# Optimization experiments

Hardware: AMD Instinct MI355X
Metric: run time of the kernel (lower is better)

Reference implementation:

```python
import jax, jax.numpy as jnp
import numpy as np

B, C, H, W = 16, 3, 512, 512
TH, TW = 32, 32  # template h, w


def setup_inputs() -> dict:
    key = jax.random.key(0)
    k1, k2 = jax.random.split(key)
    im = jax.random.normal(k1, (B, C, H, W), dtype=jnp.float32)
    template = jax.random.normal(k2, (B, C, TH, TW), dtype=jnp.float32)
    return {"im": im, "template": template}


def _integral(x):
    # double cumsum -> integral image
    return jnp.cumsum(jnp.cumsum(x, axis=-1), axis=-2)


def _rect_sum(int_im, out_h, out_w, rh, rw):
    # Sum over rh x rw rectangles centered on each pixel. Because the gather
    # indices in the torch code form contiguous ranges, advanced indexing
    # reduces to 4 static slices of the integral image.
    return (int_im[..., :out_h, :out_w] + int_im[..., rh:, rw:]
            - int_im[..., :out_h, rw:] - int_im[..., rh:, :out_w])


def _ncc(im, template):
    Hh, Ww = im.shape[-2], im.shape[-1]
    th, tw = template.shape[-2], template.shape[-1]
    padWl = (tw - 1) // 2
    padWr = padWl + 1 - tw % 2
    padHt = (th - 1) // 2
    padHb = padHt + 1 - th % 2
    rh = padHt + padHb + 1  # rectangle height (== th for even th)
    rw = padWl + padWr + 1
    pad2d = ((0, 0), (0, 0), (padHt + 1, padHb), (padWl + 1, padWr))

    # local-mean centering via integral image
    rect = _rect_sum(_integral(jnp.pad(im, pad2d)), Hh, Ww, rh, rw)
    im_c = im - rect / (th * tw)
    t_c = template - template.mean(axis=(-2, -1), keepdims=True)

    # local energy via second integral image over squared centered image
    rect2 = _rect_sum(_integral(jnp.pad(im_c * im_c, pad2d)), Hh, Ww, rh, rw)
    energy = jnp.sqrt(jnp.clip(rect2, 0.0))
    t_norm = jnp.sqrt(jnp.sum(t_c * t_c, axis=(-2, -1), keepdims=True))

    # FFT cross-correlation (padding='same')
    ph = Hh + th - th % 2 - Hh % 2
    pw = Ww + tw - tw % 2 - Ww % 2
    f_im = jnp.fft.rfft2(im_c / energy, s=(ph, pw))
    f_t = jnp.fft.rfft2(jnp.flip(t_c / t_norm, axis=(-2, -1)), s=(ph, pw))
    full = jnp.fft.irfft2(f_im * f_t, s=(ph, pw))
    hH, hW = th // 2, tw // 2
    return full[..., hH:hH + Hh, hW:hW + Ww]


def reference(im, template):
    return _ncc(im, template)
```

## Files before the change

kernel.cpp:

```cpp
#include <hip/hip_runtime.h>
#include <hip/hip_bf16.h>
#include <math.h>

#define HH 512
#define WW 512
#define BC 48
#define GW 544
#define GH 545
#define PST (GH * GW)

#define ROWB 384
#define COPYSTRIDE 6208
#define BUFSTRIDE (2 * COPYSTRIDE)
#define LDSBYTES (2 * BUFSTRIDE)

#define SIMS 98

typedef __bf16 v8bf __attribute__((ext_vector_type(8)));
typedef float v16f __attribute__((ext_vector_type(16)));

__global__ __launch_bounds__(256) void k_template(const float* __restrict__ t,
                                                  __hip_bfloat16* __restrict__ tn)
{
    __shared__ float red[256];
    const int bc = blockIdx.x, tid = threadIdx.x;
    const float* tp = t + bc * 1024;
    float v0 = tp[tid], v1 = tp[tid + 256], v2 = tp[tid + 512], v3 = tp[tid + 768];
    red[tid] = v0 + v1 + v2 + v3;
    __syncthreads();
    for (int sft = 128; sft > 0; sft >>= 1) {
        if (tid < sft) red[tid] += red[tid + sft];
        __syncthreads();
    }
    float mean = red[0] * (1.0f / 1024.0f);
    __syncthreads();
    float c0 = v0 - mean, c1 = v1 - mean, c2 = v2 - mean, c3 = v3 - mean;
    red[tid] = c0 * c0 + c1 * c1 + c2 * c2 + c3 * c3;
    __syncthreads();
    for (int sft = 128; sft > 0; sft >>= 1) {
        if (tid < sft) red[tid] += red[tid + sft];
        __syncthreads();
    }
    float norm = sqrtf(red[0]);
    __hip_bfloat16* o = tn + bc * 1024;
    o[tid] = __float2bfloat16(c0 / norm);
    o[tid + 256] = __float2bfloat16(c1 / norm);
    o[tid + 512] = __float2bfloat16(c2 / norm);
    o[tid + 768] = __float2bfloat16(c3 / norm);
}

__global__ __launch_bounds__(256) void k_center2(const float* __restrict__ im,
                                                 __hip_bfloat16* __restrict__ T0)
{
    __shared__ __hip_bfloat16 sim[159 * SIMS];
    __shared__ float hs[159 * 64];
    const int j0 = blockIdx.x * 64;
    const int i0 = blockIdx.y * 128;
    const int plane = blockIdx.z;
    const int tid = threadIdx.x;
    const size_t iplane = (size_t)plane * HH * WW;
    const size_t gplane = (size_t)plane * PST;

    for (int k = tid; k < 159 * 96; k += 256) {
        int r = k / 96, c = k - r * 96;
        int gi = i0 + r - 15, gj = j0 + c - 16;
        float v = (gi >= 0 && gi < HH && gj >= 0 && gj < WW)
                      ? im[iplane + (size_t)gi * WW + gj] : 0.f;
        sim[r * SIMS + c] = __float2bfloat16(v);
    }
    __syncthreads();

    if (tid < 159) {
        const __hip_bfloat16* sr = sim + tid * SIMS;
        float s0 = 0.f;
#pragma unroll
        for (int c = 1; c <= 32; c++) s0 += __bfloat162float(sr[c]);
        hs[tid * 64] = s0;
        for (int j = 1; j < 64; j++) {
            s0 += __bfloat162float(sr[j + 32]) - __bfloat162float(sr[j]);
            hs[tid * 64 + j] = s0;
        }
    }
    __syncthreads();

    const int tc = tid & 63;
    const int lr0 = (tid >> 6) * 32;
    float run = 0.f;
#pragma unroll
    for (int d = 0; d < 32; d++) run += hs[(lr0 + d) * 64 + tc];
    for (int rr = 0; rr < 32; rr++) {
        int lr = lr0 + rr;
        int gi = i0 + lr;
        float imv = __bfloat162float(sim[(lr + 15) * SIMS + tc + 16]);
        float val = imv - run * (1.0f / 1024.0f);
        T0[gplane + (size_t)(16 + gi) * GW + 16 + j0 + tc] = __float2bfloat16(val);
        if (rr < 31) run += hs[(lr + 32) * 64 + tc] - hs[lr * 64 + tc];
    }
    if (blockIdx.x == 0) {
        for (int k = tid; k < 128 * 16; k += 256) {
            int rr = k >> 4, x = k & 15;
            T0[gplane + (size_t)(16 + i0 + rr) * GW + x] = __float2bfloat16(0.f);
        }
    }
    if (blockIdx.x == 7) {
        for (int k = tid; k < 128 * 16; k += 256) {
            int rr = k >> 4, x = k & 15;
            T0[gplane + (size_t)(16 + i0 + rr) * GW + 528 + x] = __float2bfloat16(0.f);
        }
    }
    if (blockIdx.x == 0 && blockIdx.y == 0) {
        for (int k = tid; k < 16 * GW; k += 256)
            T0[gplane + k] = __float2bfloat16(0.f);
    }
    if (blockIdx.x == 0 && blockIdx.y == 3) {
        size_t b = gplane + (size_t)528 * GW;
        for (int k = tid; k < 17 * GW; k += 256)
            T0[b + k] = __float2bfloat16(0.f);
    }
}

__global__ __launch_bounds__(256) void k_norm2(const __hip_bfloat16* __restrict__ T0,
                                               __hip_bfloat16* __restrict__ G0,
                                               __hip_bfloat16* __restrict__ G1)
{
    __shared__ __hip_bfloat16 sim[159 * SIMS];
    __shared__ float hs[159 * 64];
    const int j0 = blockIdx.x * 64;
    const int i0 = blockIdx.y * 128;
    const int plane = blockIdx.z;
    const int tid = threadIdx.x;
    const size_t gplane = (size_t)plane * PST;

    for (int k = tid; k < 159 * 96; k += 256) {
        int r = k / 96, c = k - r * 96;
        sim[r * SIMS + c] = T0[gplane + (size_t)(i0 + 1 + r) * GW + j0 + c];
    }
    __syncthreads();

    if (tid < 159) {
        const __hip_bfloat16* sr = sim + tid * SIMS;
        float s0 = 0.f;
#pragma unroll
        for (int c = 1; c <= 32; c++) {
            float v = __bfloat162float(sr[c]);
            s0 += v * v;
        }
        hs[tid * 64] = s0;
        for (int j = 1; j < 64; j++) {
            float a = __bfloat162float(sr[j + 32]);
            float b = __bfloat162float(sr[j]);
            s0 += a * a - b * b;
            hs[tid * 64 + j] = s0;
        }
    }
    __syncthreads();

    const int tc = tid & 63;
    const int lr0 = (tid >> 6) * 32;
    float run = 0.f;
#pragma unroll
    for (int d = 0; d < 32; d++) run += hs[(lr0 + d) * 64 + tc];
    for (int rr = 0; rr < 32; rr++) {
        int lr = lr0 + rr;
        int gi = i0 + lr;
        int c = j0 + tc;
        float e = sqrtf(fmaxf(run, 0.f));
        float v = __bfloat162float(sim[(lr + 15) * SIMS + tc + 16]) / e;
        __hip_bfloat16 w = __float2bfloat16(v);
        size_t pr = gplane + (size_t)(16 + gi) * GW;
        G0[pr + 16 + c] = w;
        G1[pr + 15 + c] = w;
        if (rr < 31) run += hs[(lr + 32) * 64 + tc] - hs[lr * 64 + tc];
    }
    if (blockIdx.x == 0) {
        for (int k = tid; k < 128 * 16; k += 256) {
            int rr = k >> 4, x = k & 15;
            size_t pr = gplane + (size_t)(16 + i0 + rr) * GW;
            G0[pr + x] = __float2bfloat16(0.f);
            if (x < 15) G1[pr + x] = __float2bfloat16(0.f);
        }
    }
    if (blockIdx.x == 7) {
        for (int k = tid; k < 128 * 17; k += 256) {
            int rr = k / 17, x = k % 17;
            size_t pr = gplane + (size_t)(16 + i0 + rr) * GW;
            G1[pr + 527 + x] = __float2bfloat16(0.f);
            if (x > 0) G0[pr + 527 + x] = __float2bfloat16(0.f);
        }
    }
    if (blockIdx.x == 0 && blockIdx.y == 0) {
        for (int k = tid; k < 16 * GW; k += 256) {
            G0[gplane + k] = __float2bfloat16(0.f);
            G1[gplane + k] = __float2bfloat16(0.f);
        }
    }
    if (blockIdx.x == 0 && blockIdx.y == 3) {
        size_t b = gplane + (size_t)528 * GW;
        for (int k = tid; k < 17 * GW; k += 256) {
            G0[b + k] = __float2bfloat16(0.f);
            G1[b + k] = __float2bfloat16(0.f);
        }
    }
}

template <int PHASE>
__device__ __forceinline__ void compute_chunk(const unsigned int* __restrict__ Lr,
                                              v8bf a0, v8bf a1,
                                              float (&C)[16],
                                              int h, int Tbase, int i0,
                                              float* outp)
{
#pragma unroll
    for (int t = 0; t < 16; ++t) {
        const unsigned int* p = Lr + PHASE * (BUFSTRIDE / 4) + t * (ROWB / 4);
        union { unsigned int u[4]; v8bf v; } B0, B1;
        B0.u[0] = p[0];  B0.u[1] = p[1];  B0.u[2] = p[2];  B0.u[3] = p[3];
        B1.u[0] = p[8];  B1.u[1] = p[9];  B1.u[2] = p[10]; B1.u[3] = p[11];
        v16f c;
#pragma unroll
        for (int q = 0; q < 16; ++q) c[q] = C[q];
        c = __builtin_amdgcn_mfma_f32_32x32x16_bf16(a1, B1.v, c, 0, 0, 0);
        c = __builtin_amdgcn_mfma_f32_32x32x16_bf16(a0, B0.v, c, 0, 0, 0);
        const int T = Tbase + t;
        if (T >= 31 && T <= 94) {
            if (h) {
                const int ret = i0 - 31 + T;
                outp[(size_t)ret * WW] = c[15];
            }
        }
        float t3  = __shfl_xor(c[3], 32);
        float t7  = __shfl_xor(c[7], 32);
        float t11 = __shfl_xor(c[11], 32);
        float t15 = __shfl_xor(c[15], 32);
        C[0]  = h ? t3  : 0.f;
        C[4]  = h ? t7  : t3;
        C[8]  = h ? t11 : t7;
        C[12] = h ? t15 : t11;
#pragma unroll
        for (int g = 0; g < 4; ++g)
#pragma unroll
            for (int k = 1; k < 4; ++k)
                C[4 * g + k] = c[4 * g + k - 1];
    }
}

__global__ __launch_bounds__(256) void k_corr_mfma(const __hip_bfloat16* __restrict__ G0,
                                                   const __hip_bfloat16* __restrict__ G1,
                                                   const __hip_bfloat16* __restrict__ Tn,
                                                   float* __restrict__ out)
{
    __shared__ __align__(16) char lds[LDSBYTES];
    const int tid = threadIdx.x;
    const int wid = tid >> 6;
    const int lane = tid & 63;
    const int n = lane & 31;
    const int h = lane >> 5;
    const int j0 = blockIdx.x * 128;
    const int j0w = j0 + wid * 32;
    const int i0 = blockIdx.y * 64;
    const int plane = blockIdx.z;

    const v8bf* tp = (const v8bf*)(Tn + (size_t)plane * 1024 + n * 32 + 8 * h);
    const v8bf a0 = tp[0];
    const v8bf a1 = tp[2];

    const int c0 = j0w + n - 15 + 8 * h;
    const int sel = c0 & 1;
    const int dbase = (32 * wid + n + 1 + 8 * h - sel) >> 1;
    const unsigned int* Lr = (const unsigned int*)(lds + sel * COPYSTRIDE) + dbase;

    const __hip_bfloat16* g0p = G0 + (size_t)plane * PST + (size_t)(i0 + 1) * GW + j0;
    const __hip_bfloat16* g1p = G1 + (size_t)plane * PST + (size_t)(i0 + 1) * GW + j0;

    const __hip_bfloat16* srcp[3];
    int ldso[3];
#pragma unroll
    for (int k = 0; k < 3; ++k) {
        int s = wid + 4 * k;
        int cp = (s >= 6) ? 1 : 0;
        int c2 = cp ? (s - 6) : s;
        int q = c2 * 1024 + lane * 16;
        int rl = q / ROWB;
        int cb = q - rl * ROWB;
        srcp[k] = (cp ? g1p : g0p) + rl * GW + (cb >> 1);
        ldso[k] = cp * COPYSTRIDE + c2 * 1024;
    }

    float C[16];
#pragma unroll
    for (int s = 0; s < 16; s++) C[s] = 0.f;

    float* outp = out + (size_t)plane * HH * WW + j0w + n;

    auto stage = [&](int R, int b) {
#pragma unroll
        for (int k = 0; k < 3; ++k) {
            __builtin_amdgcn_global_load_lds(
                (const __attribute__((address_space(1))) void*)(srcp[k] + (size_t)R * GW),
                (__attribute__((address_space(3))) void*)(lds + b * BUFSTRIDE + ldso[k]),
                16, 0, 0);
        }
    };

    stage(0, 0);
    stage(16, 1);
    __syncthreads();

    for (int k2 = 0; k2 < 3; ++k2) {
        compute_chunk<0>(Lr, a0, a1, C, h, 32 * k2, i0, outp);
        __syncthreads();
        if (k2 < 2) stage(32 * k2 + 32, 0);
        compute_chunk<1>(Lr, a0, a1, C, h, 32 * k2 + 16, i0, outp);
        __syncthreads();
        if (k2 < 2) stage(32 * k2 + 48, 1);
    }
}

extern "C" void kernel_launch(void* const* d_in, const int* in_sizes, int n_in,
                              void* d_out, int out_size, void* d_ws, size_t ws_size,
                              hipStream_t stream)
{
    const float* im = (const float*)d_in[0];
    const float* tmpl = (const float*)d_in[1];
    float* outp = (float*)d_out;
    __hip_bfloat16* T0 = (__hip_bfloat16*)d_out;
    __hip_bfloat16* G0 = (__hip_bfloat16*)d_ws;
    __hip_bfloat16* G1 = G0 + (size_t)BC * PST;
    __hip_bfloat16* Tn = G1 + (size_t)BC * PST;

    k_template<<<48, 256, 0, stream>>>(tmpl, Tn);
    k_center2<<<dim3(8, 4, BC), 256, 0, stream>>>(im, T0);
    k_norm2<<<dim3(8, 4, BC), 256, 0, stream>>>(T0, G0, G1);
    k_corr_mfma<<<dim3(4, 8, BC), 256, 0, stream>>>(G0, G1, Tn, outp);
}
```

Measured before the change: 299.6 us.

## Replace LDS staging in MFMA correlation with direct global register prefetch

The correlation kernel no longer stages image rows into shared memory with global_load_lds and block barriers. Each lane now loads its B-operand vectors straight from global memory into a rotating register ring six rows deep, fully unrolled over the 96 rows. This removes LDS traffic and __syncthreads stalls, at the cost of more VGPRs and redundant, possibly unaligned global/L2 reads across overlapping lanes.

Result: no change. 303.4 us (+1.3%).

```diff
diff --git a/kernel.cpp b/kernel.cpp
--- a/kernel.cpp
+++ b/kernel.cpp
@@ -8,11 +8,6 @@
 #define GW 544
 #define GH 545
 #define PST (GH * GW)
-
-#define ROWB 384
-#define COPYSTRIDE 6208
-#define BUFSTRIDE (2 * COPYSTRIDE)
-#define LDSBYTES (2 * BUFSTRIDE)
 
 #define SIMS 98
 
@@ -203,25 +198,59 @@
     }
 }
 
-template <int PHASE>
-__device__ __forceinline__ void compute_chunk(const unsigned int* __restrict__ Lr,
-                                              v8bf a0, v8bf a1,
-                                              float (&C)[16],
-                                              int h, int Tbase, int i0,
-                                              float* outp)
-{
-#pragma unroll
-    for (int t = 0; t < 16; ++t) {
-        const unsigned int* p = Lr + PHASE * (BUFSTRIDE / 4) + t * (ROWB / 4);
-        union { unsigned int u[4]; v8bf v; } B0, B1;
-        B0.u[0] = p[0];  B0.u[1] = p[1];  B0.u[2] = p[2];  B0.u[3] = p[3];
-        B1.u[0] = p[8];  B1.u[1] = p[9];  B1.u[2] = p[10]; B1.u[3] = p[11];
+#define PFD 6
+
+__global__ __launch_bounds__(256) void k_corr_mfma(const __hip_bfloat16* __restrict__ G0,
+                                                   const __hip_bfloat16* __restrict__ G1,
+                                                   const __hip_bfloat16* __restrict__ Tn,
+                                                   float* __restrict__ out)
+{
+    const int tid = threadIdx.x;
+    const int wid = tid >> 6;
+    const int lane = tid & 63;
+    const int n = lane & 31;
+    const int h = lane >> 5;
+    const int j0w = blockIdx.x * 128 + wid * 32;
+    const int i0 = blockIdx.y * 64;
+    const int plane = blockIdx.z;
+
+    const v8bf* tp = (const v8bf*)(Tn + (size_t)plane * 1024 + n * 32 + 8 * h);
+    const v8bf a0 = tp[0];
+    const v8bf a1 = tp[2];
+
+    const int c0 = j0w + n - 15 + 8 * h;
+    const int sel = c0 & 1;
+    const __hip_bfloat16* gsel = sel ? G1 : G0;
+    const __hip_bfloat16* pb = gsel + (size_t)plane * PST
+                             + (size_t)(i0 + 1) * GW + 16 + (c0 - sel);
+
+    float C[16];
+#pragma unroll
+    for (int s = 0; s < 16; s++) C[s] = 0.f;
+
+    float* outp = out + (size_t)plane * HH * WW + j0w + n;
+
+    v8bf qb0[PFD], qb1[PFD];
+#pragma unroll
+    for (int d = 0; d < PFD; ++d) {
+        const v8bf* rp = (const v8bf*)(pb + (size_t)d * GW);
+        qb0[d] = rp[0];
+        qb1[d] = rp[2];
+    }
+
+#pragma unroll
+    for (int T = 0; T < 96; ++T) {
+        const int slot = T % PFD;
         v16f c;
 #pragma unroll
         for (int q = 0; q < 16; ++q) c[q] = C[q];
-        c = __builtin_amdgcn_mfma_f32_32x32x16_bf16(a1, B1.v, c, 0, 0, 0);
-        c = __builtin_amdgcn_mfma_f32_32x32x16_bf16(a0, B0.v, c, 0, 0, 0);
-        const int T = Tbase + t;
+        c = __builtin_amdgcn_mfma_f32_32x32x16_bf16(a1, qb1[slot], c, 0, 0, 0);
+        c = __builtin_amdgcn_mfma_f32_32x32x16_bf16(a0, qb0[slot], c, 0, 0, 0);
+        if (T + PFD < 96) {
+            const v8bf* rp = (const v8bf*)(pb + (size_t)(T + PFD) * GW);
+            qb0[slot] = rp[0];
+            qb1[slot] = rp[2];
+        }
         if (T >= 31 && T <= 94) {
             if (h) {
                 const int ret = i0 - 31 + T;
@@ -244,78 +273,6 @@
     }
 }
 
-__global__ __launch_bounds__(256) void k_corr_mfma(const __hip_bfloat16* __restrict__ G0,
-                                                   const __hip_bfloat16* __restrict__ G1,
-                                                   const __hip_bfloat16* __restrict__ Tn,
-                                                   float* __restrict__ out)
-{
-    __shared__ __align__(16) char lds[LDSBYTES];
-    const int tid = threadIdx.x;
-    const int wid = tid >> 6;
-    const int lane = tid & 63;
-    const int n = lane & 31;
-    const int h = lane >> 5;
-    const int j0 = blockIdx.x * 128;
-    const int j0w = j0 + wid * 32;
-    const int i0 = blockIdx.y * 64;
-    const int plane = blockIdx.z;
-
-    const v8bf* tp = (const v8bf*)(Tn + (size_t)plane * 1024 + n * 32 + 8 * h);
-    const v8bf a0 = tp[0];
-    const v8bf a1 = tp[2];
-
-    const int c0 = j0w + n - 15 + 8 * h;
-    const int sel = c0 & 1;
-    const int dbase = (32 * wid + n + 1 + 8 * h - sel) >> 1;
-    const unsigned int* Lr = (const unsigned int*)(lds + sel * COPYSTRIDE) + dbase;
-
-    const __hip_bfloat16* g0p = G0 + (size_t)plane * PST + (size_t)(i0 + 1) * GW + j0;
-    const __hip_bfloat16* g1p = G1 + (size_t)plane * PST + (size_t)(i0 + 1) * GW + j0;
-
-    const __hip_bfloat16* srcp[3];
-    int ldso[3];
-#pragma unroll
-    for (int k = 0; k < 3; ++k) {
-        int s = wid + 4 * k;
-        int cp = (s >= 6) ? 1 : 0;
-        int c2 = cp ? (s - 6) : s;
-        int q = c2 * 1024 + lane * 16;
-        int rl = q / ROWB;
-        int cb = q - rl * ROWB;
-        srcp[k] = (cp ? g1p : g0p) + rl * GW + (cb >> 1);
-        ldso[k] = cp * COPYSTRIDE + c2 * 1024;
-    }
-
-    float C[16];
-#pragma unroll
-    for (int s = 0; s < 16; s++) C[s] = 0.f;
-
-    float* outp = out + (size_t)plane * HH * WW + j0w + n;
-
-    auto stage = [&](int R, int b) {
-#pragma unroll
-        for (int k = 0; k < 3; ++k) {
-            __builtin_amdgcn_global_load_lds(
-                (const __attribute__((address_space(1))) void*)(srcp[k] + (size_t)R * GW),
-                (__attribute__((address_space(3))) void*)(lds + b * BUFSTRIDE + ldso[k]),
-                16, 0, 0);
-        }
-    };
-
-    stage(0, 0);
-    stage(16, 1);
-    __syncthreads();
-
-    for (int k2 = 0; k2 < 3; ++k2) {
-        compute_chunk<0>(Lr, a0, a1, C, h, 32 * k2, i0, outp);
-        __syncthreads();
-        if (k2 < 2) stage(32 * k2 + 32, 0);
-        compute_chunk<1>(Lr, a0, a1, C, h, 32 * k2 + 16, i0, outp);
-        __syncthreads();
-        if (k2 < 2) stage(32 * k2 + 48, 1);
-    }
-}
-
 extern "C" void kernel_launch(void* const* d_in, const int* in_sizes, int n_in,
                               void* d_out, int out_size, void* d_ws, size_t ws_size,
                               hipStream_t stream)
```
